# Kernel tuning notes

Measured on AMD Instinct MI355X. Metric: run time of the kernel, lower is better.

Reference implementation:

```python
import jax, jax.numpy as jnp
import numpy as np

N_NODES = 50000
N_EDGES = 500000
LN_EPS = 1e-5
COS_EPS = 1e-8


def _layernorm(x, g, b):
    # LayerNorm over last dim, affine
    mu = jnp.mean(x, axis=-1, keepdims=True)
    var = jnp.mean((x - mu) ** 2, axis=-1, keepdims=True)
    return (x - mu) * jax.lax.rsqrt(var + LN_EPS) * g + b


def _filter_conv(x, W, g, b, Bw, Bb, src, dst, heads, ch, concat):
    """One FilterGraphConv layer (eval mode, aggr='add').
    src/dst: raw edge_index rows (no self loops)."""
    N = x.shape[0]
    E = src.shape[0]
    # mu_neb = matmul(adj_t, x, reduce='mean'); adj row=src, col=dst
    deg = jax.ops.segment_sum(jnp.ones((E,), x.dtype), src, num_segments=N)
    mu = jax.ops.segment_sum(x[dst], src, num_segments=N) / jnp.maximum(deg, 1.0)[:, None]
    # x_l = lin_l(x).view(N, H, C); layernorm per head-channel block
    xl = (x @ W).reshape(N, heads, ch)
    xl_ln = _layernorm(xl, g, b)
    # add self loops (inputs guaranteed self-loop-free)
    loop = jnp.arange(N, dtype=src.dtype)
    s2 = jnp.concatenate([src, loop])
    d2 = jnp.concatenate([dst, loop])
    # cosine-similarity attention on neighborhood means
    a = mu[s2]
    c = mu[d2]
    denom = jnp.maximum(jnp.linalg.norm(a, axis=-1) * jnp.linalg.norm(c, axis=-1), COS_EPS)
    alpha = jnp.sum(a * c, axis=-1) / denom  # [E+N]
    # message = LN(x_j) * alpha, scatter-add to destination
    msg = xl_ln[s2] * alpha[:, None, None]  # [E+N, H, C]
    out = jax.ops.segment_sum(msg, d2, num_segments=N)  # [N, H, C]
    out = out.reshape(N, heads * ch) if concat else out.mean(axis=1)
    # bias linear applied to the layer input
    return out + x @ Bw + Bb


def setup_inputs() -> dict:
    key = jax.random.key(0)
    ks = jax.random.split(key, 16)
    N, E = N_NODES, N_EDGES
    x = jax.random.normal(ks[0], (N, 128), jnp.float32)
    src = jax.random.randint(ks[1], (E,), 0, N, dtype=jnp.int32)
    off = jax.random.randint(ks[2], (E,), 1, N, dtype=jnp.int32)
    dst = (src + off) % N  # guaranteed no self loops
    edge_index = jnp.stack([src, dst])

    def glorot(k, shape):
        lim = np.sqrt(6.0 / (shape[0] + shape[1]))
        return jax.random.uniform(k, shape, jnp.float32, -lim, lim)

    return {
        'x': x, 'edge_index': edge_index,
        'W0': glorot(ks[3], (128, 256)), 'g0': jnp.ones((64,)), 'b0': jnp.zeros((64,)),
        'B0': glorot(ks[4], (128, 256)) * 0.1, 'bb0': jax.random.normal(ks[5], (256,)) * 0.01,
        'W1': glorot(ks[6], (256, 256)), 'g1': jnp.ones((64,)), 'b1': jnp.zeros((64,)),
        'B1': glorot(ks[7], (256, 256)) * 0.1, 'bb1': jax.random.normal(ks[8], (256,)) * 0.01,
        'W2': glorot(ks[9], (256, 40)), 'g2': jnp.ones((40,)), 'b2': jnp.zeros((40,)),
        'B2': glorot(ks[10], (256, 1)) * 0.1, 'bb2': jax.random.normal(ks[11], (1,)) * 0.01,
    }


def reference(x, edge_index, W0, g0, b0, B0, bb0, W1, g1, b1, B1, bb1, W2, g2, b2, B2, bb2):
    src, dst = edge_index[0], edge_index[1]
    h = _filter_conv(x, W0, g0, b0, B0, bb0, src, dst, heads=4, ch=64, concat=True)
    h = jax.nn.elu(h)
    h = _filter_conv(h, W1, g1, b1, B1, bb1, src, dst, heads=4, ch=64, concat=True)
    h = jax.nn.elu(h)
    out = _filter_conv(h, W2, g2, b2, B2, bb2, src, dst, heads=1, ch=40, concat=False)
    return jax.nn.log_softmax(out, axis=-1)
```

## Files before the change

kernel.cpp:

```cpp
#include <hip/hip_runtime.h>
#include <math.h>

#define LN_EPS 1e-5f
#define COS_EPS 1e-8f

typedef short bf16x8 __attribute__((ext_vector_type(8)));
typedef float f32x4 __attribute__((ext_vector_type(4)));

static __device__ __forceinline__ unsigned short f2bf(float f) {
    unsigned u = __float_as_uint(f);
    u = u + 0x7FFFu + ((u >> 16) & 1u);
    return (unsigned short)(u >> 16);
}
static __device__ __forceinline__ float bf2f(short s) {
    return __uint_as_float(((unsigned)(unsigned short)s) << 16);
}

static __device__ __forceinline__ unsigned f2i8(float f) {
    int i = (int)rintf(f);
    i = max(-127, min(127, i));
    return (unsigned)i & 0xffu;
}

static __device__ __forceinline__ int dot4i8(int a, int b, int c) {
#if defined(__has_builtin) && __has_builtin(__builtin_amdgcn_sdot4)
    return __builtin_amdgcn_sdot4(a, b, c, false);
#else
    int s = c;
#pragma unroll
    for (int k = 0; k < 4; ++k) {
        int av = (a << (24 - 8 * k)) >> 24;
        int bv = (b << (24 - 8 * k)) >> 24;
        s += av * bv;
    }
    return s;
#endif
}

template<int EPL>
static __device__ __forceinline__ void loadrow(const short* __restrict__ p, float* r) {
    if constexpr (EPL == 4) {
        short4 v = *reinterpret_cast<const short4*>(p);
        r[0] = bf2f(v.x); r[1] = bf2f(v.y); r[2] = bf2f(v.z); r[3] = bf2f(v.w);
    } else {
        short2 v = *reinterpret_cast<const short2*>(p);
        r[0] = bf2f(v.x); r[1] = bf2f(v.y);
    }
}
template<int EPL>
static __device__ __forceinline__ void storerow(short* __restrict__ p, const float* m) {
    if constexpr (EPL == 4) {
        short4 v;
        v.x = (short)f2bf(m[0]); v.y = (short)f2bf(m[1]);
        v.z = (short)f2bf(m[2]); v.w = (short)f2bf(m[3]);
        *reinterpret_cast<short4*>(p) = v;
    } else {
        short2 v;
        v.x = (short)f2bf(m[0]); v.y = (short)f2bf(m[1]);
        *reinterpret_cast<short2*>(p) = v;
    }
}

template<int EPL>
static __device__ __forceinline__ int loadpk(const unsigned char* __restrict__ p) {
    if constexpr (EPL == 4) return (int)*reinterpret_cast<const unsigned*>(p);
    else                    return (int)*reinterpret_cast<const unsigned short*>(p);
}

__global__ void count_deg(const int* __restrict__ src, const int* __restrict__ dst,
                          int* __restrict__ deg_src, int* __restrict__ deg_dst, int E) {
    int e = blockIdx.x * blockDim.x + threadIdx.x;
    if (e < E) {
        atomicAdd(&deg_src[src[e]], 1);
        atomicAdd(&deg_dst[dst[e]], 1);
    }
}

__global__ void scan_phase1(const int* __restrict__ degA, const int* __restrict__ degB,
                            int* __restrict__ rpA, int* __restrict__ rpB,
                            int* __restrict__ bsA, int* __restrict__ bsB, int n, int nb) {
    __shared__ int sdata[256];
    int bid = blockIdx.x;
    const int* deg; int* rp; int* bs; int seg;
    if (bid < nb) { deg = degA; rp = rpA; bs = bsA; seg = bid; }
    else          { deg = degB; rp = rpB; bs = bsB; seg = bid - nb; }
    int i = seg * 256 + threadIdx.x;
    int v = (i < n) ? deg[i] : 0;
    sdata[threadIdx.x] = v;
    __syncthreads();
    for (int off = 1; off < 256; off <<= 1) {
        int t = (threadIdx.x >= off) ? sdata[threadIdx.x - off] : 0;
        __syncthreads();
        sdata[threadIdx.x] += t;
        __syncthreads();
    }
    if (i < n) rp[i] = sdata[threadIdx.x] - v;
    if (threadIdx.x == 255) bs[seg] = sdata[255];
}

__global__ void scan_phase2(int* __restrict__ bsA, int* __restrict__ bsB, int nb,
                            int* __restrict__ rpA, int* __restrict__ rpB, int n) {
    __shared__ int sdata[256];
    __shared__ int s_carry;
    for (int arr = 0; arr < 2; ++arr) {
        int* bs = arr ? bsB : bsA;
        int* rp = arr ? rpB : rpA;
        if (threadIdx.x == 0) s_carry = 0;
        __syncthreads();
        for (int base = 0; base < nb; base += 256) {
            int i = base + threadIdx.x;
            int v = (i < nb) ? bs[i] : 0;
            sdata[threadIdx.x] = v;
            __syncthreads();
            for (int off = 1; off < 256; off <<= 1) {
                int t = (threadIdx.x >= off) ? sdata[threadIdx.x - off] : 0;
                __syncthreads();
                sdata[threadIdx.x] += t;
                __syncthreads();
            }
            if (i < nb) bs[i] = s_carry + sdata[threadIdx.x] - v;
            __syncthreads();
            if (threadIdx.x == 255) s_carry += sdata[255];
            __syncthreads();
        }
        if (threadIdx.x == 0) rp[n] = s_carry;
        __syncthreads();
    }
}

__global__ void scan_phase3(int* __restrict__ rpA, int* __restrict__ rpB,
                            const int* __restrict__ bsA, const int* __restrict__ bsB,
                            int* __restrict__ curA, int* __restrict__ curB, int n, int nb) {
    int bid = blockIdx.x;
    if (bid < nb) {
        int i = bid * 256 + threadIdx.x;
        if (i < n) { int v = rpA[i] + bsA[bid]; rpA[i] = v; curA[i] = v; }
    } else {
        int seg = bid - nb;
        int i = seg * 256 + threadIdx.x;
        if (i < n) { int v = rpB[i] + bsB[seg]; rpB[i] = v; curB[i] = v; }
    }
}

__global__ void fill_csr(const int* __restrict__ src, const int* __restrict__ dst,
                         int* __restrict__ cur_src, int* __restrict__ cur_dst,
                         int* __restrict__ CSRS, int* __restrict__ SRCd, int E) {
    int e = blockIdx.x * blockDim.x + threadIdx.x;
    if (e < E) {
        int s = src[e], d = dst[e];
        int p = atomicAdd(&cur_src[s], 1);
        int q = atomicAdd(&cur_dst[d], 1);
        __builtin_nontemporal_store(d, CSRS + p);
        __builtin_nontemporal_store(s, SRCd + q);
    }
}

__global__ void cast_bf16(const float* __restrict__ X, short* __restrict__ Y, int n4) {
    int i = blockIdx.x * blockDim.x + threadIdx.x;
    if (i >= n4) return;
    float4 v = reinterpret_cast<const float4*>(X)[i];
    short4 o;
    o.x = (short)f2bf(v.x); o.y = (short)f2bf(v.y);
    o.z = (short)f2bf(v.z); o.w = (short)f2bf(v.w);
    reinterpret_cast<short4*>(Y)[i] = o;
}

__global__ void pack_w(const float* __restrict__ W, short* __restrict__ Wp,
                       int KT, int NCT_total, int ct_base, int nct_local, int ncols) {
    int idx = blockIdx.x * blockDim.x + threadIdx.x;
    int total = KT * nct_local * 512;
    if (idx >= total) return;
    int j = idx & 7;
    int l = (idx >> 3) & 63;
    int t = idx >> 9;
    int ctl = t % nct_local;
    int kt = t / nct_local;
    int k = kt * 32 + (l >> 4) * 8 + j;
    int col = ctl * 16 + (l & 15);
    float v = (col < ncols) ? W[(size_t)k * ncols + col] : 0.f;
    Wp[(((size_t)kt * NCT_total + ct_base + ctl) * 64 + l) * 8 + j] = (short)f2bf(v);
}

template<int KT, int NCT, int NCT_A, int MODE>
__global__ __launch_bounds__(512) void mfma_gemm_v5(const short* __restrict__ Xb,
                                                    const short* __restrict__ Wp,
                                                    short* __restrict__ XL,
                                                    short* __restrict__ XBb,
                                                    const float* __restrict__ g,
                                                    const float* __restrict__ b,
                                                    int M, int CoA) {
    __shared__ short bsm[NCT * 512];
    const int K = KT * 32;
    int lane = threadIdx.x & 63;
    int wave = threadIdx.x >> 6;
    size_t row0 = ((size_t)blockIdx.x * 8 + wave) * 16;
    bool active = row0 < (size_t)M;
    const short* arow = Xb + (row0 + (lane & 15)) * K + (lane >> 4) * 8;

    f32x4 acc[NCT];
#pragma unroll
    for (int ct = 0; ct < NCT; ++ct) {
        f32x4 z = {0.f, 0.f, 0.f, 0.f};
        acc[ct] = z;
    }

#pragma unroll 1
    for (int kt = 0; kt < KT; ++kt) {
        __syncthreads();
        const int4* wsrc = reinterpret_cast<const int4*>(Wp + (size_t)kt * NCT * 512);
        int4* wdst = reinterpret_cast<int4*>(bsm);
        for (int i = threadIdx.x; i < NCT * 64; i += 512) wdst[i] = wsrc[i];
        __syncthreads();
        if (active) {
            bf16x8 a = *reinterpret_cast<const bf16x8*>(arow + kt * 32);
#pragma unroll
            for (int ct = 0; ct < NCT; ++ct) {
                bf16x8 bv = *reinterpret_cast<const bf16x8*>(bsm + ct * 512 + lane * 8);
                acc[ct] = __builtin_amdgcn_mfma_f32_16x16x32_bf16(a, bv, acc[ct], 0, 0, 0);
            }
        }
    }
    if (!active) return;

    int c0 = lane & 15;
    int r0 = (lane >> 4) * 4;
    if constexpr (MODE == 1) {
        float gg[4], bv[4];
#pragma unroll
        for (int m = 0; m < 4; ++m) {
            gg[m] = g[m * 16 + c0];
            bv[m] = b[m * 16 + c0];
        }
#pragma unroll
        for (int h = 0; h < NCT_A / 4; ++h) {
#pragma unroll
            for (int j = 0; j < 4; ++j) {
                float s = acc[4*h+0][j] + acc[4*h+1][j] + acc[4*h+2][j] + acc[4*h+3][j];
                s += __shfl_xor(s, 1, 64); s += __shfl_xor(s, 2, 64);
                s += __shfl_xor(s, 4, 64); s += __shfl_xor(s, 8, 64);
                float mu_ = s * 0.015625f;
                float d0 = acc[4*h+0][j] - mu_, d1 = acc[4*h+1][j] - mu_;
                float d2 = acc[4*h+2][j] - mu_, d3 = acc[4*h+3][j] - mu_;
                float s2 = d0*d0 + d1*d1 + d2*d2 + d3*d3;
                s2 += __shfl_xor(s2, 1, 64); s2 += __shfl_xor(s2, 2, 64);
                s2 += __shfl_xor(s2, 4, 64); s2 += __shfl_xor(s2, 8, 64);
                float rs = rsqrtf(s2 * 0.015625f + LN_EPS);
                size_t row = row0 + r0 + j;
                short* rowp = XL + row * 256 + c0;
                rowp[(4*h+0)*16] = (short)f2bf(d0 * rs * gg[0] + bv[0]);
                rowp[(4*h+1)*16] = (short)f2bf(d1 * rs * gg[1] + bv[1]);
                rowp[(4*h+2)*16] = (short)f2bf(d2 * rs * gg[2] + bv[2]);
                rowp[(4*h+3)*16] = (short)f2bf(d3 * rs * gg[3] + bv[3]);
            }
        }
#pragma unroll
        for (int ct = NCT_A; ct < NCT; ++ct) {
#pragma unroll
            for (int j = 0; j < 4; ++j) {
                size_t row = row0 + r0 + j;
                XBb[row * 256 + (ct - NCT_A) * 16 + c0] = (short)f2bf(acc[ct][j]);
            }
        }
    } else if constexpr (MODE == 2) {
        bool valid[NCT];
        float gg[NCT], bv[NCT];
#pragma unroll
        for (int ct = 0; ct < NCT; ++ct) {
            int col = ct * 16 + c0;
            valid[ct] = col < 40;
            gg[ct] = valid[ct] ? g[col] : 0.f;
            bv[ct] = valid[ct] ? b[col] : 0.f;
        }
#pragma unroll
        for (int j = 0; j < 4; ++j) {
            float s = 0.f;
#pragma unroll
            for (int ct = 0; ct < NCT; ++ct) s += valid[ct] ? acc[ct][j] : 0.f;
            s += __shfl_xor(s, 1, 64); s += __shfl_xor(s, 2, 64);
            s += __shfl_xor(s, 4, 64); s += __shfl_xor(s, 8, 64);
            float mu_ = s * 0.025f;
            float d[NCT];
            float s2 = 0.f;
#pragma unroll
            for (int ct = 0; ct < NCT; ++ct) {
                d[ct] = valid[ct] ? (acc[ct][j] - mu_) : 0.f;
                s2 += d[ct] * d[ct];
            }
            s2 += __shfl_xor(s2, 1, 64); s2 += __shfl_xor(s2, 2, 64);
            s2 += __shfl_xor(s2, 4, 64); s2 += __shfl_xor(s2, 8, 64);
            float rs = rsqrtf(s2 * 0.025f + LN_EPS);
            size_t row = row0 + r0 + j;
#pragma unroll
            for (int ct = 0; ct < NCT; ++ct) {
                int col = ct * 16 + c0;
                if (valid[ct]) XL[row * 40 + col] = (short)f2bf(d[ct] * rs * gg[ct] + bv[ct]);
            }
        }
    } else {
#pragma unroll
        for (int ct = 0; ct < NCT; ++ct) {
            int col = ct * 16 + c0;
#pragma unroll
            for (int j = 0; j < 4; ++j) {
                size_t row = row0 + r0 + j;
                if (ct < NCT_A) {
                    if (col < CoA) XL[row * CoA + col] = (short)f2bf(acc[ct][j]);
                } else {
                    XBb[row * 256 + (col - NCT_A * 16)] = (short)f2bf(acc[ct][j]);
                }
            }
        }
    }
}


template<int EPL>
__global__ void mu_norm_v5(const short* __restrict__ Xb, const int* __restrict__ rp,
                           const int* __restrict__ CSRS, unsigned char* __restrict__ MUn,
                           float* __restrict__ NRM, int N) {
    int n = (blockIdx.x * blockDim.x + threadIdx.x) >> 6;
    int lane = threadIdx.x & 63;
    if (n >= N) return;
    const int Fin = EPL * 64;
    int j0 = rp[n], j1 = rp[n + 1];
    float acc[EPL];
#pragma unroll
    for (int k = 0; k < EPL; ++k) acc[k] = 0.f;
    int j = j0;
    for (; j + 8 <= j1; j += 8) {
        int dd[8];
#pragma unroll
        for (int u = 0; u < 8; ++u) dd[u] = CSRS[j + u];
        float r[8][EPL];
#pragma unroll
        for (int u = 0; u < 8; ++u)
            loadrow<EPL>(Xb + (size_t)dd[u] * Fin + lane * EPL, r[u]);
#pragma unroll
        for (int u = 0; u < 8; ++u)
#pragma unroll
            for (int k = 0; k < EPL; ++k) acc[k] += r[u][k];
    }
    for (; j < j1; ++j) {
        int d = CSRS[j];
        float r[EPL];
        loadrow<EPL>(Xb + (size_t)d * Fin + lane * EPL, r);
#pragma unroll
        for (int k = 0; k < EPL; ++k) acc[k] += r[k];
    }
    float inv = 1.f / fmaxf((float)(j1 - j0), 1.f);
    float m[EPL];
    float s = 0.f;
#pragma unroll
    for (int k = 0; k < EPL; ++k) { m[k] = acc[k] * inv; s += m[k] * m[k]; }
    for (int msk = 32; msk > 0; msk >>= 1) s += __shfl_xor(s, msk, 64);
    float nrm = sqrtf(s);
    float innv = 127.f / fmaxf(nrm, 1e-8f);
    unsigned pk = 0;
#pragma unroll
    for (int k = 0; k < EPL; ++k) pk |= f2i8(m[k] * innv) << (8 * k);
    if constexpr (EPL == 4)
        *reinterpret_cast<unsigned*>(MUn + (size_t)n * Fin + lane * 4) = pk;
    else
        *reinterpret_cast<unsigned short*>(MUn + (size_t)n * Fin + lane * 2) =
            (unsigned short)pk;
    if (lane == 0) NRM[n] = nrm;
}

template<int EPLM>
__global__ void scatter_fused_elu(const unsigned char* __restrict__ MUn,
                                  const short* __restrict__ XLN,
                                  const int* __restrict__ rp_dst, const int* __restrict__ SRCd,
                                  const float* __restrict__ NRM,
                                  const short* __restrict__ XB, const float* __restrict__ bb,
                                  short* __restrict__ Yb, int N) {
    const float ISC = 1.f / 16129.f;
    int n = (blockIdx.x * blockDim.x + threadIdx.x) >> 6;
    int lane = threadIdx.x & 63;
    if (n >= N) return;
    const int FinM = EPLM * 64;
    int mn_i = loadpk<EPLM>(MUn + (size_t)n * FinM + lane * EPLM);
    int j0 = rp_dst[n], j1 = rp_dst[n + 1];
    float acc[4] = {0.f, 0.f, 0.f, 0.f};
    int j = j0;
    for (; j + 4 <= j1; j += 4) {
        int ss[4];
#pragma unroll
        for (int u = 0; u < 4; ++u) ss[u] = SRCd[j + u];
        int ms[4];
        float xl[4][4];
#pragma unroll
        for (int u = 0; u < 4; ++u)
            ms[u] = loadpk<EPLM>(MUn + (size_t)ss[u] * FinM + lane * EPLM);
#pragma unroll
        for (int u = 0; u < 4; ++u)
            loadrow<4>(XLN + (size_t)ss[u] * 256 + lane * 4, xl[u]);
        int t[4];
#pragma unroll
        for (int u = 0; u < 4; ++u) t[u] = dot4i8(mn_i, ms[u], 0);
#pragma unroll
        for (int u = 0; u < 4; ++u)
            for (int msk = 32; msk > 0; msk >>= 1) t[u] += __shfl_xor(t[u], msk, 64);
#pragma unroll
        for (int u = 0; u < 4; ++u) {
            float al = (float)t[u] * ISC;
#pragma unroll
            for (int k = 0; k < 4; ++k) acc[k] += xl[u][k] * al;
        }
    }
    for (; j < j1; ++j) {
        int s = SRCd[j];
        int ms = loadpk<EPLM>(MUn + (size_t)s * FinM + lane * EPLM);
        float xl[4];
        loadrow<4>(XLN + (size_t)s * 256 + lane * 4, xl);
        int t = dot4i8(mn_i, ms, 0);
        for (int msk = 32; msk > 0; msk >>= 1) t += __shfl_xor(t, msk, 64);
        float al = (float)t * ISC;
#pragma unroll
        for (int k = 0; k < 4; ++k) acc[k] += xl[k] * al;
    }
    float nn = NRM[n], n2 = nn * nn;
    float aself = n2 / fmaxf(n2, COS_EPS);
    float rs[4];
    loadrow<4>(XLN + (size_t)n * 256 + lane * 4, rs);
#pragma unroll
    for (int k = 0; k < 4; ++k) acc[k] += rs[k] * aself;

    float xb[4], o[4];
    loadrow<4>(XB + (size_t)n * 256 + lane * 4, xb);
    float4 bv = *reinterpret_cast<const float4*>(bb + lane * 4);
    o[0] = acc[0] + xb[0] + bv.x; o[1] = acc[1] + xb[1] + bv.y;
    o[2] = acc[2] + xb[2] + bv.z; o[3] = acc[3] + xb[3] + bv.w;
#pragma unroll
    for (int k = 0; k < 4; ++k) o[k] = (o[k] > 0.f) ? o[k] : expm1f(o[k]);
    storerow<4>(Yb + (size_t)n * 256 + lane * 4, o);
}

__global__ void scatter_final_fused(const unsigned char* __restrict__ MUn,
                                    const short* __restrict__ XLN,
                                    const int* __restrict__ rp_dst, const int* __restrict__ SRCd,
                                    const float* __restrict__ NRM, float* __restrict__ OUT,
                                    int N) {
    const float ISC = 1.f / 16129.f;
    int n = (blockIdx.x * blockDim.x + threadIdx.x) >> 6;
    int lane = threadIdx.x & 63;
    if (n >= N) return;
    bool act = lane < 40;
    int mn_i = loadpk<4>(MUn + (size_t)n * 256 + lane * 4);
    int j0 = rp_dst[n], j1 = rp_dst[n + 1];
    float acc = 0.f;
    int j = j0;
    for (; j + 4 <= j1; j += 4) {
        int ss[4];
#pragma unroll
        for (int u = 0; u < 4; ++u) ss[u] = SRCd[j + u];
        int ms[4];
        float xl[4];
#pragma unroll
        for (int u = 0; u < 4; ++u)
            ms[u] = loadpk<4>(MUn + (size_t)ss[u] * 256 + lane * 4);
#pragma unroll
        for (int u = 0; u < 4; ++u)
            xl[u] = act ? bf2f(XLN[(size_t)ss[u] * 40 + lane]) : 0.f;
        int t[4];
#pragma unroll
        for (int u = 0; u < 4; ++u) t[u] = dot4i8(mn_i, ms[u], 0);
#pragma unroll
        for (int u = 0; u < 4; ++u)
            for (int msk = 32; msk > 0; msk >>= 1) t[u] += __shfl_xor(t[u], msk, 64);
#pragma unroll
        for (int u = 0; u < 4; ++u) acc += xl[u] * ((float)t[u] * ISC);
    }
    for (; j < j1; ++j) {
        int s = SRCd[j];
        int ms = loadpk<4>(MUn + (size_t)s * 256 + lane * 4);
        float xl = act ? bf2f(XLN[(size_t)s * 40 + lane]) : 0.f;
        int t = dot4i8(mn_i, ms, 0);
        for (int msk = 32; msk > 0; msk >>= 1) t += __shfl_xor(t, msk, 64);
        acc += xl * ((float)t * ISC);
    }
    float nn = NRM[n], n2 = nn * nn;
    float aself = n2 / fmaxf(n2, COS_EPS);
    acc += (act ? bf2f(XLN[(size_t)n * 40 + lane]) : 0.f) * aself;

    float v = act ? acc : -INFINITY;
    float mx = v;
    for (int msk = 32; msk > 0; msk >>= 1) mx = fmaxf(mx, __shfl_xor(mx, msk, 64));
    float ex = act ? expf(v - mx) : 0.f;
    float se = ex;
    for (int msk = 32; msk > 0; msk >>= 1) se += __shfl_xor(se, msk, 64);
    if (act) OUT[(size_t)n * 40 + lane] = v - mx - logf(se);
}

extern "C" void kernel_launch(void* const* d_in, const int* in_sizes, int n_in,
                              void* d_out, int out_size, void* d_ws, size_t ws_size,
                              hipStream_t stream) {
    const float* x   = (const float*)d_in[0];
    const int*   ei  = (const int*)d_in[1];
    const float* W0  = (const float*)d_in[2];
    const float* g0  = (const float*)d_in[3];
    const float* b0  = (const float*)d_in[4];
    const float* B0  = (const float*)d_in[5];
    const float* bb0 = (const float*)d_in[6];
    const float* W1  = (const float*)d_in[7];
    const float* g1  = (const float*)d_in[8];
    const float* b1  = (const float*)d_in[9];
    const float* B1  = (const float*)d_in[10];
    const float* bb1 = (const float*)d_in[11];
    const float* W2  = (const float*)d_in[12];
    const float* g2  = (const float*)d_in[13];
    const float* b2  = (const float*)d_in[14];
    float* out = (float*)d_out;

    const int N = in_sizes[0] / 128;
    const int E = in_sizes[1] / 2;
    const int* src = ei;
    const int* dst = ei + E;

    char* ws = (char*)d_ws;
    size_t off = 0;
    auto alloc = [&](size_t bytes) -> void* {
        void* p = ws + off;
        off += (bytes + 255) & ~(size_t)255;
        return p;
    };
    int* deg_src     = (int*)alloc((size_t)N * 4);
    int* deg_dst     = (int*)alloc((size_t)N * 4);
    int* rp_src      = (int*)alloc((size_t)(N + 1) * 4);
    int* rp_dst      = (int*)alloc((size_t)(N + 1) * 4);
    int* cur_src     = (int*)alloc((size_t)N * 4);
    int* cur_dst     = (int*)alloc((size_t)N * 4);
    int* bs_src      = (int*)alloc((size_t)1024 * 4);
    int* bs_dst      = (int*)alloc((size_t)1024 * 4);
    int* CSRS        = (int*)alloc((size_t)E * 4);
    int* SRCd        = (int*)alloc((size_t)E * 4);
    float* NRM       = (float*)alloc((size_t)N * 4);
    unsigned char* MUn = (unsigned char*)alloc((size_t)N * 256);
    short* XBb       = (short*)alloc((size_t)N * 256 * 2);
    short* XLb       = (short*)alloc((size_t)N * 256 * 2);
    short* Xb_a      = (short*)alloc((size_t)N * 256 * 2);
    short* Xb_b      = (short*)alloc((size_t)N * 256 * 2);
    short* Wp        = (short*)alloc((size_t)8 * 32 * 64 * 8 * 2);
    (void)ws_size;

    hipMemsetAsync(deg_src, 0, (size_t)N * 4, stream);
    hipMemsetAsync(deg_dst, 0, (size_t)N * 4, stream);
    int egrid = (E + 255) / 256;
    count_deg<<<egrid, 256, 0, stream>>>(src, dst, deg_src, deg_dst, E);
    int nb = (N + 255) / 256;
    scan_phase1<<<2 * nb, 256, 0, stream>>>(deg_src, deg_dst, rp_src, rp_dst,
                                            bs_src, bs_dst, N, nb);
    scan_phase2<<<1, 256, 0, stream>>>(bs_src, bs_dst, nb, rp_src, rp_dst, N);
    scan_phase3<<<2 * nb, 256, 0, stream>>>(rp_src, rp_dst, bs_src, bs_dst,
                                            cur_src, cur_dst, N, nb);
    fill_csr<<<egrid, 256, 0, stream>>>(src, dst, cur_src, cur_dst, CSRS, SRCd, E);

    {
        int n4 = (N * 128) / 4;
        cast_bf16<<<(n4 + 255) / 256, 256, 0, stream>>>(x, Xb_a, n4);
    }

    int wgridN = (N * 64 + 255) / 256;
    int ggrid  = (N + 127) / 128;

    mu_norm_v5<2><<<wgridN, 256, 0, stream>>>(Xb_a, rp_src, CSRS, MUn, NRM, N);
    {
        int tot = 4 * 16 * 512;
        pack_w<<<(tot + 255) / 256, 256, 0, stream>>>(W0, Wp, 4, 32, 0, 16, 256);
        pack_w<<<(tot + 255) / 256, 256, 0, stream>>>(B0, Wp, 4, 32, 16, 16, 256);
    }
    mfma_gemm_v5<4, 32, 16, 1><<<ggrid, 512, 0, stream>>>(Xb_a, Wp, XLb, XBb,
                                                          g0, b0, N, 256);
    scatter_fused_elu<2><<<wgridN, 256, 0, stream>>>(MUn, XLb, rp_dst, SRCd, NRM,
                                                     XBb, bb0, Xb_b, N);

    mu_norm_v5<4><<<wgridN, 256, 0, stream>>>(Xb_b, rp_src, CSRS, MUn, NRM, N);
    {
        int tot = 8 * 16 * 512;
        pack_w<<<(tot + 255) / 256, 256, 0, stream>>>(W1, Wp, 8, 32, 0, 16, 256);
        pack_w<<<(tot + 255) / 256, 256, 0, stream>>>(B1, Wp, 8, 32, 16, 16, 256);
    }
    mfma_gemm_v5<8, 32, 16, 1><<<ggrid, 512, 0, stream>>>(Xb_b, Wp, XLb, XBb,
                                                          g1, b1, N, 256);
    scatter_fused_elu<4><<<wgridN, 256, 0, stream>>>(MUn, XLb, rp_dst, SRCd, NRM,
                                                     XBb, bb1, Xb_a, N);

    mu_norm_v5<4><<<wgridN, 256, 0, stream>>>(Xb_a, rp_src, CSRS, MUn, NRM, N);
    {
        int tot = 8 * 3 * 512;
        pack_w<<<(tot + 255) / 256, 256, 0, stream>>>(W2, Wp, 8, 3, 0, 3, 40);
    }
    mfma_gemm_v5<8, 3, 3, 2><<<ggrid, 512, 0, stream>>>(Xb_a, Wp, XLb, nullptr,
                                                        g2, b2, N, 40);
    scatter_final_fused<<<wgridN, 256, 0, stream>>>(MUn, XLb, rp_dst, SRCd, NRM, out, N);
}
```

Before: 632.1 us.

## Merge GEMM and neighbor-mean kernels into one launch with block-range dispatch

The per-layer MFMA GEMM and the mu_norm neighborhood-mean kernel become one kernel. The first ngemm blocks run the GEMM and the remaining blocks compute mean, norm and int8 quantization. The two independent phases can then run concurrently on the GPU and fill each other's idle time, and launches are fewer. All weight packing moves to the start into separate per-layer buffers so it is out of the dependency chain. The risk is that the blocks are heterogeneous: the mu-norm path must now use 512-thread blocks and share the GEMM kernel's LDS and register allocation, which may lower occupancy for the gather work.

```diff
diff --git a/kernel.cpp b/kernel.cpp
--- a/kernel.cpp
+++ b/kernel.cpp
@@ -181,189 +181,175 @@
     Wp[(((size_t)kt * NCT_total + ct_base + ctl) * 64 + l) * 8 + j] = (short)f2bf(v);
 }
 
-template<int KT, int NCT, int NCT_A, int MODE>
-__global__ __launch_bounds__(512) void mfma_gemm_v5(const short* __restrict__ Xb,
-                                                    const short* __restrict__ Wp,
-                                                    short* __restrict__ XL,
-                                                    short* __restrict__ XBb,
-                                                    const float* __restrict__ g,
-                                                    const float* __restrict__ b,
-                                                    int M, int CoA) {
+template<int KT, int NCT, int NCT_A, int MODE, int EPL>
+__global__ __launch_bounds__(512) void fused_gemm_mu(const short* __restrict__ Xb,
+                                                     const short* __restrict__ Wp,
+                                                     short* __restrict__ XL,
+                                                     short* __restrict__ XBb,
+                                                     const float* __restrict__ g,
+                                                     const float* __restrict__ b,
+                                                     const int* __restrict__ rp,
+                                                     const int* __restrict__ CSRS,
+                                                     unsigned char* __restrict__ MUn,
+                                                     float* __restrict__ NRM,
+                                                     int N, int ngemm) {
     __shared__ short bsm[NCT * 512];
-    const int K = KT * 32;
-    int lane = threadIdx.x & 63;
-    int wave = threadIdx.x >> 6;
-    size_t row0 = ((size_t)blockIdx.x * 8 + wave) * 16;
-    bool active = row0 < (size_t)M;
-    const short* arow = Xb + (row0 + (lane & 15)) * K + (lane >> 4) * 8;
-
-    f32x4 acc[NCT];
-#pragma unroll
-    for (int ct = 0; ct < NCT; ++ct) {
-        f32x4 z = {0.f, 0.f, 0.f, 0.f};
-        acc[ct] = z;
-    }
+    int tid = threadIdx.x;
+    int lane = tid & 63;
+    if ((int)blockIdx.x < ngemm) {
+        const int K = KT * 32;
+        int wave = tid >> 6;
+        size_t row0 = ((size_t)blockIdx.x * 8 + wave) * 16;
+        bool active = row0 < (size_t)N;
+        const short* arow = Xb + (row0 + (lane & 15)) * K + (lane >> 4) * 8;
+
+        f32x4 acc[NCT];
+#pragma unroll
+        for (int ct = 0; ct < NCT; ++ct) {
+            f32x4 z = {0.f, 0.f, 0.f, 0.f};
+            acc[ct] = z;
+        }
 
 #pragma unroll 1
-    for (int kt = 0; kt < KT; ++kt) {
-        __syncthreads();
-        const int4* wsrc = reinterpret_cast<const int4*>(Wp + (size_t)kt * NCT * 512);
-        int4* wdst = reinterpret_cast<int4*>(bsm);
-        for (int i = threadIdx.x; i < NCT * 64; i += 512) wdst[i] = wsrc[i];
-        __syncthreads();
-        if (active) {
-            bf16x8 a = *reinterpret_cast<const bf16x8*>(arow + kt * 32);
+        for (int kt = 0; kt < KT; ++kt) {
+            __syncthreads();
+            const int4* wsrc = reinterpret_cast<const int4*>(Wp + (size_t)kt * NCT * 512);
+            int4* wdst = reinterpret_cast<int4*>(bsm);
+            for (int i = tid; i < NCT * 64; i += 512) wdst[i] = wsrc[i];
+            __syncthreads();
+            if (active) {
+                bf16x8 a = *reinterpret_cast<const bf16x8*>(arow + kt * 32);
+#pragma unroll
+                for (int ct = 0; ct < NCT; ++ct) {
+                    bf16x8 bv = *reinterpret_cast<const bf16x8*>(bsm + ct * 512 + lane * 8);
+                    acc[ct] = __builtin_amdgcn_mfma_f32_16x16x32_bf16(a, bv, acc[ct], 0, 0, 0);
+                }
+            }
+        }
+        if (!active) return;
+
+        int c0 = lane & 15;
+        int r0 = (lane >> 4) * 4;
+        if constexpr (MODE == 1) {
+            float gg[4], bv[4];
+#pragma unroll
+            for (int m = 0; m < 4; ++m) {
+                gg[m] = g[m * 16 + c0];
+                bv[m] = b[m * 16 + c0];
+            }
+#pragma unroll
+            for (int h = 0; h < NCT_A / 4; ++h) {
+#pragma unroll
+                for (int j = 0; j < 4; ++j) {
+                    float s = acc[4*h+0][j] + acc[4*h+1][j] + acc[4*h+2][j] + acc[4*h+3][j];
+                    s += __shfl_xor(s, 1, 64); s += __shfl_xor(s, 2, 64);
+                    s += __shfl_xor(s, 4, 64); s += __shfl_xor(s, 8, 64);
+                    float mu_ = s * 0.015625f;
+                    float d0 = acc[4*h+0][j] - mu_, d1 = acc[4*h+1][j] - mu_;
+                    float d2 = acc[4*h+2][j] - mu_, d3 = acc[4*h+3][j] - mu_;
+                    float s2 = d0*d0 + d1*d1 + d2*d2 + d3*d3;
+                    s2 += __shfl_xor(s2, 1, 64); s2 += __shfl_xor(s2, 2, 64);
+                    s2 += __shfl_xor(s2, 4, 64); s2 += __shfl_xor(s2, 8, 64);
+                    float rs = rsqrtf(s2 * 0.015625f + LN_EPS);
+                    size_t row = row0 + r0 + j;
+                    short* rowp = XL + row * 256 + c0;
+                    rowp[(4*h+0)*16] = (short)f2bf(d0 * rs * gg[0] + bv[0]);
+                    rowp[(4*h+1)*16] = (short)f2bf(d1 * rs * gg[1] + bv[1]);
+                    rowp[(4*h+2)*16] = (short)f2bf(d2 * rs * gg[2] + bv[2]);
+                    rowp[(4*h+3)*16] = (short)f2bf(d3 * rs * gg[3] + bv[3]);
+                }
+            }
+#pragma unroll
+            for (int ct = NCT_A; ct < NCT; ++ct) {
+#pragma unroll
+                for (int j = 0; j < 4; ++j) {
+                    size_t row = row0 + r0 + j;
+                    XBb[row * 256 + (ct - NCT_A) * 16 + c0] = (short)f2bf(acc[ct][j]);
+                }
+            }
+        } else if constexpr (MODE == 2) {
+            bool valid[NCT];
+            float gg[NCT], bv[NCT];
 #pragma unroll
             for (int ct = 0; ct < NCT; ++ct) {
-                bf16x8 bv = *reinterpret_cast<const bf16x8*>(bsm + ct * 512 + lane * 8);
-                acc[ct] = __builtin_amdgcn_mfma_f32_16x16x32_bf16(a, bv, acc[ct], 0, 0, 0);
-            }
-        }
-    }
-    if (!active) return;
-
-    int c0 = lane & 15;
-    int r0 = (lane >> 4) * 4;
-    if constexpr (MODE == 1) {
-        float gg[4], bv[4];
-#pragma unroll
-        for (int m = 0; m < 4; ++m) {
-            gg[m] = g[m * 16 + c0];
-            bv[m] = b[m * 16 + c0];
-        }
-#pragma unroll
-        for (int h = 0; h < NCT_A / 4; ++h) {
+                int col = ct * 16 + c0;
+                valid[ct] = col < 40;
+                gg[ct] = valid[ct] ? g[col] : 0.f;
+                bv[ct] = valid[ct] ? b[col] : 0.f;
+            }
 #pragma unroll
             for (int j = 0; j < 4; ++j) {
-                float s = acc[4*h+0][j] + acc[4*h+1][j] + acc[4*h+2][j] + acc[4*h+3][j];
+                float s = 0.f;
+#pragma unroll
+                for (int ct = 0; ct < NCT; ++ct) s += valid[ct] ? acc[ct][j] : 0.f;
                 s += __shfl_xor(s, 1, 64); s += __shfl_xor(s, 2, 64);
                 s += __shfl_xor(s, 4, 64); s += __shfl_xor(s, 8, 64);
-                float mu_ = s * 0.015625f;
-                float d0 = acc[4*h+0][j] - mu_, d1 = acc[4*h+1][j] - mu_;
-                float d2 = acc[4*h+2][j] - mu_, d3 = acc[4*h+3][j] - mu_;
-                float s2 = d0*d0 + d1*d1 + d2*d2 + d3*d3;
+                float mu_ = s * 0.025f;
+                float d[NCT];
+                float s2 = 0.f;
+#pragma unroll
+                for (int ct = 0; ct < NCT; ++ct) {
+                    d[ct] = valid[ct] ? (acc[ct][j] - mu_) : 0.f;
+                    s2 += d[ct] * d[ct];
+                }
                 s2 += __shfl_xor(s2, 1, 64); s2 += __shfl_xor(s2, 2, 64);
                 s2 += __shfl_xor(s2, 4, 64); s2 += __shfl_xor(s2, 8, 64);
-                float rs = rsqrtf(s2 * 0.015625f + LN_EPS);
+                float rs = rsqrtf(s2 * 0.025f + LN_EPS);
                 size_t row = row0 + r0 + j;
-                short* rowp = XL + row * 256 + c0;
-                rowp[(4*h+0)*16] = (short)f2bf(d0 * rs * gg[0] + bv[0]);
-                rowp[(4*h+1)*16] = (short)f2bf(d1 * rs * gg[1] + bv[1]);
-                rowp[(4*h+2)*16] = (short)f2bf(d2 * rs * gg[2] + bv[2]);
-                rowp[(4*h+3)*16] = (short)f2bf(d3 * rs * gg[3] + bv[3]);
-            }
-        }
-#pragma unroll
-        for (int ct = NCT_A; ct < NCT; ++ct) {
-#pragma unroll
-            for (int j = 0; j < 4; ++j) {
-                size_t row = row0 + r0 + j;
-                XBb[row * 256 + (ct - NCT_A) * 16 + c0] = (short)f2bf(acc[ct][j]);
-            }
-        }
-    } else if constexpr (MODE == 2) {
-        bool valid[NCT];
-        float gg[NCT], bv[NCT];
-#pragma unroll
-        for (int ct = 0; ct < NCT; ++ct) {
-            int col = ct * 16 + c0;
-            valid[ct] = col < 40;
-            gg[ct] = valid[ct] ? g[col] : 0.f;
-            bv[ct] = valid[ct] ? b[col] : 0.f;
-        }
-#pragma unroll
-        for (int j = 0; j < 4; ++j) {
-            float s = 0.f;
-#pragma unroll
-            for (int ct = 0; ct < NCT; ++ct) s += valid[ct] ? acc[ct][j] : 0.f;
-            s += __shfl_xor(s, 1, 64); s += __shfl_xor(s, 2, 64);
-            s += __shfl_xor(s, 4, 64); s += __shfl_xor(s, 8, 64);
-            float mu_ = s * 0.025f;
-            float d[NCT];
-            float s2 = 0.f;
-#pragma unroll
-            for (int ct = 0; ct < NCT; ++ct) {
-                d[ct] = valid[ct] ? (acc[ct][j] - mu_) : 0.f;
-                s2 += d[ct] * d[ct];
-            }
-            s2 += __shfl_xor(s2, 1, 64); s2 += __shfl_xor(s2, 2, 64);
-            s2 += __shfl_xor(s2, 4, 64); s2 += __shfl_xor(s2, 8, 64);
-            float rs = rsqrtf(s2 * 0.025f + LN_EPS);
-            size_t row = row0 + r0 + j;
-#pragma unroll
-            for (int ct = 0; ct < NCT; ++ct) {
-                int col = ct * 16 + c0;
-                if (valid[ct]) XL[row * 40 + col] = (short)f2bf(d[ct] * rs * gg[ct] + bv[ct]);
+#pragma unroll
+                for (int ct = 0; ct < NCT; ++ct) {
+                    int col = ct * 16 + c0;
+                    if (valid[ct]) XL[row * 40 + col] = (short)f2bf(d[ct] * rs * gg[ct] + bv[ct]);
+                }
             }
         }
     } else {
-#pragma unroll
-        for (int ct = 0; ct < NCT; ++ct) {
-            int col = ct * 16 + c0;
-#pragma unroll
-            for (int j = 0; j < 4; ++j) {
-                size_t row = row0 + r0 + j;
-                if (ct < NCT_A) {
-                    if (col < CoA) XL[row * CoA + col] = (short)f2bf(acc[ct][j]);
-                } else {
-                    XBb[row * 256 + (col - NCT_A * 16)] = (short)f2bf(acc[ct][j]);
-                }
-            }
-        }
-    }
-}
-
-
-template<int EPL>
-__global__ void mu_norm_v5(const short* __restrict__ Xb, const int* __restrict__ rp,
-                           const int* __restrict__ CSRS, unsigned char* __restrict__ MUn,
-                           float* __restrict__ NRM, int N) {
-    int n = (blockIdx.x * blockDim.x + threadIdx.x) >> 6;
-    int lane = threadIdx.x & 63;
-    if (n >= N) return;
-    const int Fin = EPL * 64;
-    int j0 = rp[n], j1 = rp[n + 1];
-    float acc[EPL];
-#pragma unroll
-    for (int k = 0; k < EPL; ++k) acc[k] = 0.f;
-    int j = j0;
-    for (; j + 8 <= j1; j += 8) {
-        int dd[8];
-#pragma unroll
-        for (int u = 0; u < 8; ++u) dd[u] = CSRS[j + u];
-        float r[8][EPL];
-#pragma unroll
-        for (int u = 0; u < 8; ++u)
-            loadrow<EPL>(Xb + (size_t)dd[u] * Fin + lane * EPL, r[u]);
-#pragma unroll
-        for (int u = 0; u < 8; ++u)
-#pragma unroll
-            for (int k = 0; k < EPL; ++k) acc[k] += r[u][k];
-    }
-    for (; j < j1; ++j) {
-        int d = CSRS[j];
-        float r[EPL];
-        loadrow<EPL>(Xb + (size_t)d * Fin + lane * EPL, r);
-#pragma unroll
-        for (int k = 0; k < EPL; ++k) acc[k] += r[k];
-    }
-    float inv = 1.f / fmaxf((float)(j1 - j0), 1.f);
-    float m[EPL];
-    float s = 0.f;
-#pragma unroll
-    for (int k = 0; k < EPL; ++k) { m[k] = acc[k] * inv; s += m[k] * m[k]; }
-    for (int msk = 32; msk > 0; msk >>= 1) s += __shfl_xor(s, msk, 64);
-    float nrm = sqrtf(s);
-    float innv = 127.f / fmaxf(nrm, 1e-8f);
-    unsigned pk = 0;
-#pragma unroll
-    for (int k = 0; k < EPL; ++k) pk |= f2i8(m[k] * innv) << (8 * k);
-    if constexpr (EPL == 4)
-        *reinterpret_cast<unsigned*>(MUn + (size_t)n * Fin + lane * 4) = pk;
-    else
-        *reinterpret_cast<unsigned short*>(MUn + (size_t)n * Fin + lane * 2) =
-            (unsigned short)pk;
-    if (lane == 0) NRM[n] = nrm;
+        int n = ((int)blockIdx.x - ngemm) * 8 + (tid >> 6);
+        if (n >= N) return;
+        const int Fin = EPL * 64;
+        int j0 = rp[n], j1 = rp[n + 1];
+        float acc[EPL];
+#pragma unroll
+        for (int k = 0; k < EPL; ++k) acc[k] = 0.f;
+        int j = j0;
+        for (; j + 8 <= j1; j += 8) {
+            int dd[8];
+#pragma unroll
+            for (int u = 0; u < 8; ++u) dd[u] = CSRS[j + u];
+            float r[8][EPL];
+#pragma unroll
+            for (int u = 0; u < 8; ++u)
+                loadrow<EPL>(Xb + (size_t)dd[u] * Fin + lane * EPL, r[u]);
+#pragma unroll
+            for (int u = 0; u < 8; ++u)
+#pragma unroll
+                for (int k = 0; k < EPL; ++k) acc[k] += r[u][k];
+        }
+        for (; j < j1; ++j) {
+            int d = CSRS[j];
+            float r[EPL];
+            loadrow<EPL>(Xb + (size_t)d * Fin + lane * EPL, r);
+#pragma unroll
+            for (int k = 0; k < EPL; ++k) acc[k] += r[k];
+        }
+        float inv = 1.f / fmaxf((float)(j1 - j0), 1.f);
+        float m[EPL];
+        float s = 0.f;
+#pragma unroll
+        for (int k = 0; k < EPL; ++k) { m[k] = acc[k] * inv; s += m[k] * m[k]; }
+        for (int msk = 32; msk > 0; msk >>= 1) s += __shfl_xor(s, msk, 64);
+        float nrm = sqrtf(s);
+        float innv = 127.f / fmaxf(nrm, 1e-8f);
+        unsigned pk = 0;
+#pragma unroll
+        for (int k = 0; k < EPL; ++k) pk |= f2i8(m[k] * innv) << (8 * k);
+        if constexpr (EPL == 4)
+            *reinterpret_cast<unsigned*>(MUn + (size_t)n * Fin + lane * 4) = pk;
+        else
+            *reinterpret_cast<unsigned short*>(MUn + (size_t)n * Fin + lane * 2) =
+                (unsigned short)pk;
+        if (lane == 0) NRM[n] = nrm;
+    }
 }
 
 template<int EPLM>
@@ -539,8 +525,25 @@
     short* XLb       = (short*)alloc((size_t)N * 256 * 2);
     short* Xb_a      = (short*)alloc((size_t)N * 256 * 2);
     short* Xb_b      = (short*)alloc((size_t)N * 256 * 2);
-    short* Wp        = (short*)alloc((size_t)8 * 32 * 64 * 8 * 2);
+    short* Wp0       = (short*)alloc((size_t)4 * 32 * 512 * 2);
+    short* Wp1       = (short*)alloc((size_t)8 * 32 * 512 * 2);
+    short* Wp2       = (short*)alloc((size_t)8 * 3 * 512 * 2);
     (void)ws_size;
+
+    {
+        int n4 = (N * 128) / 4;
+        cast_bf16<<<(n4 + 255) / 256, 256, 0, stream>>>(x, Xb_a, n4);
+    }
+    {
+        int t0 = 4 * 16 * 512;
+        pack_w<<<(t0 + 255) / 256, 256, 0, stream>>>(W0, Wp0, 4, 32, 0, 16, 256);
+        pack_w<<<(t0 + 255) / 256, 256, 0, stream>>>(B0, Wp0, 4, 32, 16, 16, 256);
+        int t1 = 8 * 16 * 512;
+        pack_w<<<(t1 + 255) / 256, 256, 0, stream>>>(W1, Wp1, 8, 32, 0, 16, 256);
+        pack_w<<<(t1 + 255) / 256, 256, 0, stream>>>(B1, Wp1, 8, 32, 16, 16, 256);
+        int t2 = 8 * 3 * 512;
+        pack_w<<<(t2 + 255) / 256, 256, 0, stream>>>(W2, Wp2, 8, 3, 0, 3, 40);
+    }
 
     hipMemsetAsync(deg_src, 0, (size_t)N * 4, stream);
     hipMemsetAsync(deg_dst, 0, (size_t)N * 4, stream);
@@ -554,42 +557,22 @@
                                             cur_src, cur_dst, N, nb);
     fill_csr<<<egrid, 256, 0, stream>>>(src, dst, cur_src, cur_dst, CSRS, SRCd, E);
 
-    {
-        int n4 = (N * 128) / 4;
-        cast_bf16<<<(n4 + 255) / 256, 256, 0, stream>>>(x, Xb_a, n4);
-    }
-
     int wgridN = (N * 64 + 255) / 256;
-    int ggrid  = (N + 127) / 128;
-
-    mu_norm_v5<2><<<wgridN, 256, 0, stream>>>(Xb_a, rp_src, CSRS, MUn, NRM, N);
-    {
-        int tot = 4 * 16 * 512;
-        pack_w<<<(tot + 255) / 256, 256, 0, stream>>>(W0, Wp, 4, 32, 0, 16, 256);
-        pack_w<<<(tot + 255) / 256, 256, 0, stream>>>(B0, Wp, 4, 32, 16, 16, 256);
-    }
-    mfma_gemm_v5<4, 32, 16, 1><<<ggrid, 512, 0, stream>>>(Xb_a, Wp, XLb, XBb,
-                                                          g0, b0, N, 256);
+    int ngemm  = (N + 127) / 128;
+    int nmu    = (N + 7) / 8;
+    int nfat   = ngemm + nmu;
+
+    fused_gemm_mu<4, 32, 16, 1, 2><<<nfat, 512, 0, stream>>>(
+        Xb_a, Wp0, XLb, XBb, g0, b0, rp_src, CSRS, MUn, NRM, N, ngemm);
     scatter_fused_elu<2><<<wgridN, 256, 0, stream>>>(MUn, XLb, rp_dst, SRCd, NRM,
                                                      XBb, bb0, Xb_b, N);
 
-    mu_norm_v5<4><<<wgridN, 256, 0, stream>>>(Xb_b, rp_src, CSRS, MUn, NRM, N);
-    {
-        int tot = 8 * 16 * 512;
-        pack_w<<<(tot + 255) / 256, 256, 0, stream>>>(W1, Wp, 8, 32, 0, 16, 256);
-        pack_w<<<(tot + 255) / 256, 256, 0, stream>>>(B1, Wp, 8, 32, 16, 16, 256);
-    }
-    mfma_gemm_v5<8, 32, 16, 1><<<ggrid, 512, 0, stream>>>(Xb_b, Wp, XLb, XBb,
-                                                          g1, b1, N, 256);
+    fused_gemm_mu<8, 32, 16, 1, 4><<<nfat, 512, 0, stream>>>(
+        Xb_b, Wp1, XLb, XBb, g1, b1, rp_src, CSRS, MUn, NRM, N, ngemm);
     scatter_fused_elu<4><<<wgridN, 256, 0, stream>>>(MUn, XLb, rp_dst, SRCd, NRM,
                                                      XBb, bb1, Xb_a, N);
 
-    mu_norm_v5<4><<<wgridN, 256, 0, stream>>>(Xb_a, rp_src, CSRS, MUn, NRM, N);
-    {
-        int tot = 8 * 3 * 512;
-        pack_w<<<(tot + 255) / 256, 256, 0, stream>>>(W2, Wp, 8, 3, 0, 3, 40);
-    }
-    mfma_gemm_v5<8, 3, 3, 2><<<ggrid, 512, 0, stream>>>(Xb_a, Wp, XLb, nullptr,
-                                                        g2, b2, N, 40);
+    fused_gemm_mu<8, 3, 3, 2, 4><<<nfat, 512, 0, stream>>>(
+        Xb_a, Wp2, XLb, nullptr, g2, b2, rp_src, CSRS, MUn, NRM, N, ngemm);
     scatter_final_fused<<<wgridN, 256, 0, stream>>>(MUn, XLb, rp_dst, SRCd, NRM, out, N);
 }
```

New measurement: 753.5 us. +19.2%, slower.
